# Kernel tuning notes

Hardware: AMD Instinct MI355X
Metric: run time of the kernel (lower is better)

Reference implementation:

```python
import jax, jax.numpy as jnp
import numpy as np

H = 4        # num_heads
R = 5        # dilation_rate
W = 49       # window_size
D = 256      # d_model // 2
B = 32
N = 4900     # must be divisible by W*R = 245


def setup_inputs() -> dict:
    key = jax.random.key(0)
    k1, k2, k3, k4, k5 = jax.random.split(key, 5)
    s = 1.0 / np.sqrt(D)
    return {
        "emb": jax.random.normal(k1, (B, N, D), dtype=jnp.float32),
        "Wq": jax.random.normal(k2, (D, D), dtype=jnp.float32) * s,
        "bq": jax.random.normal(k3, (D,), dtype=jnp.float32) * s,
        "Wo": jax.random.normal(k4, (D, D), dtype=jnp.float32) * s,
        "bo": jax.random.normal(k5, (D,), dtype=jnp.float32) * s,
    }


def reference(emb, Wq, bq, Wo, bo):
    b, n, d = emb.shape
    dh = d // H
    g = n // (W * R)  # number of segments
    # Original forward uses q_proj for q, k AND v (faithful to source bug).
    q = emb @ Wq.T + bq  # [B, N, D]
    # Dilated local windows: token index = g*(W*R) + i*R + r.
    # Tokens sharing (segment g, dilation offset r) attend densely over i in [0, W).
    x = q.reshape(b, g, W, R, H, dh)
    scale = jnp.asarray(dh, q.dtype) ** -0.5
    scores = jnp.einsum("bgirhd,bgjrhd->bgrhij", x, x) * scale  # [B,G,R,H,W,W]
    attn = jax.nn.softmax(scores, axis=-1)
    out = jnp.einsum("bgrhij,bgjrhd->bgirhd", attn, x)  # [B,G,W,R,H,dh]
    out = out.reshape(b, n, d)
    return out @ Wo.T + bo
```

## Files before the change

kernel.cpp:

```cpp
#include <hip/hip_runtime.h>
#include <hip/hip_bf16.h>
#include <math.h>

#define NH     4
#define RD     5
#define WW     49
#define DM     256
#define BATCH  32
#define NTOK   4900
#define GSEG   20
#define SEG    245

typedef short bf16x8 __attribute__((ext_vector_type(8)));
typedef short bf16x4 __attribute__((ext_vector_type(4)));
typedef float f32x4  __attribute__((ext_vector_type(4)));

__device__ __forceinline__ short f2bf(float f) {
    union { __hip_bfloat16 h; short s; } u;
    u.h = __float2bfloat16(f);
    return u.s;
}

__device__ __forceinline__ void gl_lds16(const void* g, void* l) {
    __builtin_amdgcn_global_load_lds(
        (const __attribute__((address_space(1))) void*)g,
        (__attribute__((address_space(3))) void*)l, 16, 0, 0);
}

__device__ __forceinline__ int qix(int row, int col) {
    return row * 256 + (col ^ ((row & 7) << 3));
}
__device__ __forceinline__ int tix(int d, int j) {
    return 64 * 256 + d * 64 + (j ^ ((d & 7) << 3));
}

__global__ __launch_bounds__(256)
void wcvt(const float* __restrict__ Wq, const float* __restrict__ Wo,
          short* __restrict__ Wqb, short* __restrict__ Wob) {
    int t = blockIdx.x * 256 + threadIdx.x;
    const float* src = (t < 16384) ? Wq : Wo;
    short* dst = (t < 16384) ? Wqb : Wob;
    int i = (t & 16383) * 4;
    float4 v = *(const float4*)(src + i);
    bf16x4 o = { f2bf(v.x), f2bf(v.y), f2bf(v.z), f2bf(v.w) };
    *(bf16x4*)(dst + i) = o;
}

__global__ __launch_bounds__(256, 2)
void fused(const float* __restrict__ emb, const short* __restrict__ Wqb,
           const float* __restrict__ bq, const short* __restrict__ Wob,
           const float* __restrict__ bo, float* __restrict__ out) {
    __shared__ __align__(16) short sm[64 * 256 + 64 * 256];
    float* As = (float*)sm;

    const int tid = threadIdx.x;
    const int wv = tid >> 6, ln = tid & 63, lc = ln & 15, lq = ln >> 4;

    const int bid = blockIdx.x;
    const int b = bid / 100;
    const int rem = bid - b * 100;
    const int g = rem / 5, r = rem - (rem / 5) * 5;
    const size_t tok0 = (size_t)b * NTOK + (size_t)g * SEG + r;
    const int wn = wv * 64;

    for (int p = wv; p < WW; p += 4)
        gl_lds16(emb + (tok0 + (size_t)p * RD) * DM +
                     (size_t)((ln ^ (p & 7)) << 2),
                 (char*)sm + p * 1024);
    __syncthreads();

    f32x4 acc[4][4] = {};
    {
        const short* br[4];
        #pragma unroll
        for (int ni = 0; ni < 4; ni++)
            br[ni] = Wqb + (size_t)(wn + ni * 16 + lc) * DM + lq * 8;
        bf16x8 wb[2][4];
        #pragma unroll
        for (int ni = 0; ni < 4; ni++) wb[0][ni] = *(const bf16x8*)(br[ni]);
        #pragma unroll
        for (int ni = 0; ni < 4; ni++) wb[1][ni] = *(const bf16x8*)(br[ni] + 32);

        #pragma unroll
        for (int ks = 0; ks < 8; ks++) {
            bf16x8 af[4];
            #pragma unroll
            for (int mi = 0; mi < 4; mi++) {
                const int t = mi * 16 + lc;
                const int clo = (ks * 8 + lq * 2) ^ (t & 7);
                float4 lo = *(const float4*)&As[t * 256 + clo * 4];
                float4 hi = *(const float4*)&As[t * 256 + (clo ^ 1) * 4];
                af[mi] = (bf16x8){ f2bf(lo.x), f2bf(lo.y), f2bf(lo.z), f2bf(lo.w),
                                   f2bf(hi.x), f2bf(hi.y), f2bf(hi.z), f2bf(hi.w) };
            }
            #pragma unroll
            for (int mi = 0; mi < 4; mi++)
                #pragma unroll
                for (int ni = 0; ni < 4; ni++)
                    acc[mi][ni] = __builtin_amdgcn_mfma_f32_16x16x32_bf16(
                        af[mi], wb[ks & 1][ni], acc[mi][ni], 0, 0, 0);
            if (ks < 6) {
                #pragma unroll
                for (int ni = 0; ni < 4; ni++)
                    wb[ks & 1][ni] = *(const bf16x8*)(br[ni] + (ks + 2) * 32);
            }
        }
    }
    __syncthreads();

    {
        float bv[4];
        #pragma unroll
        for (int ni = 0; ni < 4; ni++) bv[ni] = bq[wn + ni * 16 + lc];
        #pragma unroll
        for (int mi = 0; mi < 4; mi++)
            #pragma unroll
            for (int rg = 0; rg < 4; rg++) {
                const int t = mi * 16 + lq * 4 + rg;
                #pragma unroll
                for (int ni = 0; ni < 4; ni++) {
                    const int col = wn + ni * 16 + lc;
                    const short s = (t < WW) ? f2bf(acc[mi][ni][rg] + bv[ni])
                                             : (short)0;
                    sm[qix(t, col)] = s;
                    sm[tix(col, t)] = s;
                }
            }
    }
    __syncthreads();

    {
        const int c0 = wn;
        bf16x8 xa[4][2];
        #pragma unroll
        for (int mi = 0; mi < 4; mi++) {
            xa[mi][0] = *(const bf16x8*)&sm[qix(mi * 16 + lc, c0 + lq * 8)];
            xa[mi][1] = *(const bf16x8*)&sm[qix(mi * 16 + lc, c0 + 32 + lq * 8)];
        }
        f32x4 sa[4][4] = {};
        #pragma unroll
        for (int mi = 0; mi < 4; mi++)
            #pragma unroll
            for (int ni = 0; ni < 4; ni++) {
                sa[mi][ni] = __builtin_amdgcn_mfma_f32_16x16x32_bf16(
                    xa[mi][0], xa[ni][0], sa[mi][ni], 0, 0, 0);
                sa[mi][ni] = __builtin_amdgcn_mfma_f32_16x16x32_bf16(
                    xa[mi][1], xa[ni][1], sa[mi][ni], 0, 0, 0);
            }
        #pragma unroll
        for (int mi = 0; mi < 4; mi++)
            #pragma unroll
            for (int ni = 0; ni < 4; ni++)
                #pragma unroll
                for (int rg = 0; rg < 4; rg++)
                    sa[mi][ni][rg] *= 0.125f;

        const int jb = lq * 4;
        #pragma unroll
        for (int ni = 0; ni < 4; ni++) {
            float m = -1e30f;
            #pragma unroll
            for (int mi = 0; mi < 4; mi++)
                #pragma unroll
                for (int rg = 0; rg < 4; rg++) {
                    const float v = (16 * mi + rg + jb < WW) ? sa[mi][ni][rg]
                                                             : -1e30f;
                    m = fmaxf(m, v);
                }
            m = fmaxf(m, __shfl_xor(m, 16));
            m = fmaxf(m, __shfl_xor(m, 32));
            float l_ = 0.f;
            #pragma unroll
            for (int mi = 0; mi < 4; mi++)
                #pragma unroll
                for (int rg = 0; rg < 4; rg++) {
                    const float e = (16 * mi + rg + jb < WW)
                                        ? __expf(sa[mi][ni][rg] - m) : 0.f;
                    sa[mi][ni][rg] = e;
                    l_ += e;
                }
            l_ += __shfl_xor(l_, 16);
            l_ += __shfl_xor(l_, 32);
            const float inv = 1.f / l_;
            const int i = 16 * ni + lc;
            #pragma unroll
            for (int mi = 0; mi < 4; mi++) {
                bf16x4 w = { f2bf(sa[mi][ni][0] * inv), f2bf(sa[mi][ni][1] * inv),
                             f2bf(sa[mi][ni][2] * inv), f2bf(sa[mi][ni][3] * inv) };
                *(bf16x4*)&sm[qix(i, c0 + 16 * mi + jb)] = w;
            }
        }
        bf16x8 pa[4][2], pb[4][2];
        #pragma unroll
        for (int mi = 0; mi < 4; mi++) {
            pa[mi][0] = *(const bf16x8*)&sm[qix(mi * 16 + lc, c0 + lq * 8)];
            pa[mi][1] = *(const bf16x8*)&sm[qix(mi * 16 + lc, c0 + 32 + lq * 8)];
        }
        #pragma unroll
        for (int ni = 0; ni < 4; ni++) {
            pb[ni][0] = *(const bf16x8*)&sm[tix(c0 + ni * 16 + lc, lq * 8)];
            pb[ni][1] = *(const bf16x8*)&sm[tix(c0 + ni * 16 + lc, 32 + lq * 8)];
        }
        f32x4 oa[4][4] = {};
        #pragma unroll
        for (int mi = 0; mi < 4; mi++)
            #pragma unroll
            for (int ni = 0; ni < 4; ni++) {
                oa[mi][ni] = __builtin_amdgcn_mfma_f32_16x16x32_bf16(
                    pa[mi][0], pb[ni][0], oa[mi][ni], 0, 0, 0);
                oa[mi][ni] = __builtin_amdgcn_mfma_f32_16x16x32_bf16(
                    pa[mi][1], pb[ni][1], oa[mi][ni], 0, 0, 0);
            }
        #pragma unroll
        for (int mi = 0; mi < 4; mi++)
            #pragma unroll
            for (int rg = 0; rg < 4; rg++) {
                const int i = mi * 16 + lq * 4 + rg;
                if (i < WW) {
                    #pragma unroll
                    for (int ni = 0; ni < 4; ni++)
                        sm[qix(i, c0 + ni * 16 + lc)] = f2bf(oa[mi][ni][rg]);
                }
            }
    }
    __syncthreads();

    {
        const short* br[4];
        #pragma unroll
        for (int ni = 0; ni < 4; ni++)
            br[ni] = Wob + (size_t)(wn + ni * 16 + lc) * DM + lq * 8;
        int trow[4];
        #pragma unroll
        for (int mi = 0; mi < 4; mi++) {
            int t = mi * 16 + lc;
            trow[mi] = (t > WW - 1) ? (WW - 1) : t;
        }
        f32x4 ac3[4][4] = {};
        bf16x8 wb[2][4];
        #pragma unroll
        for (int ni = 0; ni < 4; ni++) wb[0][ni] = *(const bf16x8*)(br[ni]);
        #pragma unroll
        for (int ni = 0; ni < 4; ni++) wb[1][ni] = *(const bf16x8*)(br[ni] + 32);

        #pragma unroll
        for (int ks = 0; ks < 8; ks++) {
            bf16x8 af[4];
            #pragma unroll
            for (int mi = 0; mi < 4; mi++)
                af[mi] = *(const bf16x8*)&sm[qix(trow[mi], ks * 32 + lq * 8)];
            #pragma unroll
            for (int mi = 0; mi < 4; mi++)
                #pragma unroll
                for (int ni = 0; ni < 4; ni++)
                    ac3[mi][ni] = __builtin_amdgcn_mfma_f32_16x16x32_bf16(
                        af[mi], wb[ks & 1][ni], ac3[mi][ni], 0, 0, 0);
            if (ks < 6) {
                #pragma unroll
                for (int ni = 0; ni < 4; ni++)
                    wb[ks & 1][ni] = *(const bf16x8*)(br[ni] + (ks + 2) * 32);
            }
        }
        float bv[4];
        #pragma unroll
        for (int ni = 0; ni < 4; ni++) bv[ni] = bo[wn + ni * 16 + lc];
        #pragma unroll
        for (int mi = 0; mi < 4; mi++)
            #pragma unroll
            for (int rg = 0; rg < 4; rg++) {
                const int t = mi * 16 + lq * 4 + rg;
                if (t < WW) {
                    float* op = out + (tok0 + (size_t)t * RD) * DM + wn;
                    #pragma unroll
                    for (int ni = 0; ni < 4; ni++)
                        op[ni * 16 + lc] = ac3[mi][ni][rg] + bv[ni];
                }
            }
    }
}

extern "C" void kernel_launch(void* const* d_in, const int* in_sizes, int n_in,
                              void* d_out, int out_size, void* d_ws, size_t ws_size,
                              hipStream_t stream) {
    const float* emb = (const float*)d_in[0];
    const float* Wq  = (const float*)d_in[1];
    const float* bq  = (const float*)d_in[2];
    const float* Wo  = (const float*)d_in[3];
    const float* bo  = (const float*)d_in[4];
    float* out = (float*)d_out;

    short* Wqb = (short*)d_ws;
    short* Wob = Wqb + DM * DM;

    wcvt<<<dim3(128), dim3(256), 0, stream>>>(Wq, Wo, Wqb, Wob);
    fused<<<dim3(BATCH * GSEG * RD), dim3(256), 0, stream>>>(
        emb, Wqb, bq, Wob, bo, out);
}
```

Baseline: 378.7 us.

## Split each block across eight waves by row halves and vectorize transposed stores

Doubles the block to 512 threads so each head's wave pair splits the 64 token rows into two halves. This covers the Q projection, the attention, and the output projection, cutting per-wave accumulator registers and raising wave count per CU. The transposed Q copy now uses a 4-element swizzle so each lane writes one bf16x4 instead of scalar stores. An extra barrier is added before the probability writes overwrite the shared Q rows. Each wave still loads the full weight slices, so global weight traffic per block doubles.

```diff
diff --git a/kernel.cpp b/kernel.cpp
--- a/kernel.cpp
+++ b/kernel.cpp
@@ -10,6 +10,7 @@
 #define NTOK   4900
 #define GSEG   20
 #define SEG    245
+#define XTB    (64 * 256)
 
 typedef short bf16x8 __attribute__((ext_vector_type(8)));
 typedef short bf16x4 __attribute__((ext_vector_type(4)));
@@ -30,8 +31,8 @@
 __device__ __forceinline__ int qix(int row, int col) {
     return row * 256 + (col ^ ((row & 7) << 3));
 }
-__device__ __forceinline__ int tix(int d, int j) {
-    return 64 * 256 + d * 64 + (j ^ ((d & 7) << 3));
+__device__ __forceinline__ int tix4(int d, int j) {
+    return XTB + d * 64 + ((((j >> 2) ^ ((d & 7) << 1)) << 2) | (j & 3));
 }
 
 __global__ __launch_bounds__(256)
@@ -46,30 +47,31 @@
     *(bf16x4*)(dst + i) = o;
 }
 
-__global__ __launch_bounds__(256, 2)
+__global__ __launch_bounds__(512, 4)
 void fused(const float* __restrict__ emb, const short* __restrict__ Wqb,
            const float* __restrict__ bq, const short* __restrict__ Wob,
            const float* __restrict__ bo, float* __restrict__ out) {
-    __shared__ __align__(16) short sm[64 * 256 + 64 * 256];
+    __shared__ __align__(16) short sm[XTB + 64 * 256];
     float* As = (float*)sm;
 
     const int tid = threadIdx.x;
     const int wv = tid >> 6, ln = tid & 63, lc = ln & 15, lq = ln >> 4;
+    const int hd = wv & 3, hf = wv >> 2;
+    const int wn = hd * 64, wm = hf * 32;
 
     const int bid = blockIdx.x;
     const int b = bid / 100;
     const int rem = bid - b * 100;
     const int g = rem / 5, r = rem - (rem / 5) * 5;
     const size_t tok0 = (size_t)b * NTOK + (size_t)g * SEG + r;
-    const int wn = wv * 64;
-
-    for (int p = wv; p < WW; p += 4)
+
+    for (int p = wv; p < WW; p += 8)
         gl_lds16(emb + (tok0 + (size_t)p * RD) * DM +
                      (size_t)((ln ^ (p & 7)) << 2),
                  (char*)sm + p * 1024);
     __syncthreads();
 
-    f32x4 acc[4][4] = {};
+    f32x4 acc[2][4] = {};
     {
         const short* br[4];
         #pragma unroll
@@ -83,10 +85,10 @@
 
         #pragma unroll
         for (int ks = 0; ks < 8; ks++) {
-            bf16x8 af[4];
-            #pragma unroll
-            for (int mi = 0; mi < 4; mi++) {
-                const int t = mi * 16 + lc;
+            bf16x8 af[2];
+            #pragma unroll
+            for (int mi = 0; mi < 2; mi++) {
+                const int t = wm + mi * 16 + lc;
                 const int clo = (ks * 8 + lq * 2) ^ (t & 7);
                 float4 lo = *(const float4*)&As[t * 256 + clo * 4];
                 float4 hi = *(const float4*)&As[t * 256 + (clo ^ 1) * 4];
@@ -94,7 +96,7 @@
                                    f2bf(hi.x), f2bf(hi.y), f2bf(hi.z), f2bf(hi.w) };
             }
             #pragma unroll
-            for (int mi = 0; mi < 4; mi++)
+            for (int mi = 0; mi < 2; mi++)
                 #pragma unroll
                 for (int ni = 0; ni < 4; ni++)
                     acc[mi][ni] = __builtin_amdgcn_mfma_f32_16x16x32_bf16(
@@ -113,113 +115,115 @@
         #pragma unroll
         for (int ni = 0; ni < 4; ni++) bv[ni] = bq[wn + ni * 16 + lc];
         #pragma unroll
-        for (int mi = 0; mi < 4; mi++)
-            #pragma unroll
-            for (int rg = 0; rg < 4; rg++) {
-                const int t = mi * 16 + lq * 4 + rg;
-                #pragma unroll
-                for (int ni = 0; ni < 4; ni++) {
-                    const int col = wn + ni * 16 + lc;
-                    const short s = (t < WW) ? f2bf(acc[mi][ni][rg] + bv[ni])
-                                             : (short)0;
-                    sm[qix(t, col)] = s;
-                    sm[tix(col, t)] = s;
-                }
-            }
+        for (int mi = 0; mi < 2; mi++) {
+            const int t0 = wm + mi * 16 + lq * 4;
+            #pragma unroll
+            for (int ni = 0; ni < 4; ni++) {
+                const int col = wn + ni * 16 + lc;
+                short s[4];
+                #pragma unroll
+                for (int rg = 0; rg < 4; rg++)
+                    s[rg] = (t0 + rg < WW) ? f2bf(acc[mi][ni][rg] + bv[ni])
+                                           : (short)0;
+                #pragma unroll
+                for (int rg = 0; rg < 4; rg++)
+                    sm[qix(t0 + rg, col)] = s[rg];
+                bf16x4 w = { s[0], s[1], s[2], s[3] };
+                *(bf16x4*)&sm[tix4(col, t0)] = w;
+            }
+        }
     }
     __syncthreads();
 
     {
         const int c0 = wn;
-        bf16x8 xa[4][2];
-        #pragma unroll
-        for (int mi = 0; mi < 4; mi++) {
-            xa[mi][0] = *(const bf16x8*)&sm[qix(mi * 16 + lc, c0 + lq * 8)];
-            xa[mi][1] = *(const bf16x8*)&sm[qix(mi * 16 + lc, c0 + 32 + lq * 8)];
-        }
-        f32x4 sa[4][4] = {};
-        #pragma unroll
-        for (int mi = 0; mi < 4; mi++)
-            #pragma unroll
-            for (int ni = 0; ni < 4; ni++) {
-                sa[mi][ni] = __builtin_amdgcn_mfma_f32_16x16x32_bf16(
-                    xa[mi][0], xa[ni][0], sa[mi][ni], 0, 0, 0);
-                sa[mi][ni] = __builtin_amdgcn_mfma_f32_16x16x32_bf16(
-                    xa[mi][1], xa[ni][1], sa[mi][ni], 0, 0, 0);
-            }
-        #pragma unroll
-        for (int mi = 0; mi < 4; mi++)
-            #pragma unroll
-            for (int ni = 0; ni < 4; ni++)
-                #pragma unroll
-                for (int rg = 0; rg < 4; rg++)
-                    sa[mi][ni][rg] *= 0.125f;
+        bf16x8 xa[4][2], xb[2][2];
+        #pragma unroll
+        for (int mj = 0; mj < 4; mj++) {
+            xa[mj][0] = *(const bf16x8*)&sm[qix(mj * 16 + lc, c0 + lq * 8)];
+            xa[mj][1] = *(const bf16x8*)&sm[qix(mj * 16 + lc, c0 + 32 + lq * 8)];
+        }
+        #pragma unroll
+        for (int ni = 0; ni < 2; ni++) {
+            xb[ni][0] = *(const bf16x8*)&sm[qix(wm + ni * 16 + lc, c0 + lq * 8)];
+            xb[ni][1] = *(const bf16x8*)&sm[qix(wm + ni * 16 + lc, c0 + 32 + lq * 8)];
+        }
+        f32x4 sa[4][2] = {};
+        #pragma unroll
+        for (int mj = 0; mj < 4; mj++)
+            #pragma unroll
+            for (int ni = 0; ni < 2; ni++) {
+                sa[mj][ni] = __builtin_amdgcn_mfma_f32_16x16x32_bf16(
+                    xa[mj][0], xb[ni][0], sa[mj][ni], 0, 0, 0);
+                sa[mj][ni] = __builtin_amdgcn_mfma_f32_16x16x32_bf16(
+                    xa[mj][1], xb[ni][1], sa[mj][ni], 0, 0, 0);
+            }
+        __syncthreads();
 
         const int jb = lq * 4;
         #pragma unroll
-        for (int ni = 0; ni < 4; ni++) {
+        for (int ni = 0; ni < 2; ni++) {
             float m = -1e30f;
             #pragma unroll
-            for (int mi = 0; mi < 4; mi++)
+            for (int mj = 0; mj < 4; mj++)
                 #pragma unroll
                 for (int rg = 0; rg < 4; rg++) {
-                    const float v = (16 * mi + rg + jb < WW) ? sa[mi][ni][rg]
-                                                             : -1e30f;
-                    m = fmaxf(m, v);
+                    sa[mj][ni][rg] *= 0.125f;
+                    if (16 * mj + jb + rg < WW) m = fmaxf(m, sa[mj][ni][rg]);
                 }
             m = fmaxf(m, __shfl_xor(m, 16));
             m = fmaxf(m, __shfl_xor(m, 32));
             float l_ = 0.f;
             #pragma unroll
-            for (int mi = 0; mi < 4; mi++)
+            for (int mj = 0; mj < 4; mj++)
                 #pragma unroll
                 for (int rg = 0; rg < 4; rg++) {
-                    const float e = (16 * mi + rg + jb < WW)
-                                        ? __expf(sa[mi][ni][rg] - m) : 0.f;
-                    sa[mi][ni][rg] = e;
+                    const float e = (16 * mj + jb + rg < WW)
+                                        ? __expf(sa[mj][ni][rg] - m) : 0.f;
+                    sa[mj][ni][rg] = e;
                     l_ += e;
                 }
             l_ += __shfl_xor(l_, 16);
             l_ += __shfl_xor(l_, 32);
             const float inv = 1.f / l_;
-            const int i = 16 * ni + lc;
-            #pragma unroll
-            for (int mi = 0; mi < 4; mi++) {
-                bf16x4 w = { f2bf(sa[mi][ni][0] * inv), f2bf(sa[mi][ni][1] * inv),
-                             f2bf(sa[mi][ni][2] * inv), f2bf(sa[mi][ni][3] * inv) };
-                *(bf16x4*)&sm[qix(i, c0 + 16 * mi + jb)] = w;
-            }
-        }
-        bf16x8 pa[4][2], pb[4][2];
-        #pragma unroll
-        for (int mi = 0; mi < 4; mi++) {
-            pa[mi][0] = *(const bf16x8*)&sm[qix(mi * 16 + lc, c0 + lq * 8)];
-            pa[mi][1] = *(const bf16x8*)&sm[qix(mi * 16 + lc, c0 + 32 + lq * 8)];
-        }
-        #pragma unroll
-        for (int ni = 0; ni < 4; ni++) {
-            pb[ni][0] = *(const bf16x8*)&sm[tix(c0 + ni * 16 + lc, lq * 8)];
-            pb[ni][1] = *(const bf16x8*)&sm[tix(c0 + ni * 16 + lc, 32 + lq * 8)];
-        }
-        f32x4 oa[4][4] = {};
-        #pragma unroll
-        for (int mi = 0; mi < 4; mi++)
-            #pragma unroll
-            for (int ni = 0; ni < 4; ni++) {
-                oa[mi][ni] = __builtin_amdgcn_mfma_f32_16x16x32_bf16(
-                    pa[mi][0], pb[ni][0], oa[mi][ni], 0, 0, 0);
-                oa[mi][ni] = __builtin_amdgcn_mfma_f32_16x16x32_bf16(
-                    pa[mi][1], pb[ni][1], oa[mi][ni], 0, 0, 0);
-            }
-        #pragma unroll
-        for (int mi = 0; mi < 4; mi++)
+            const int i = wm + ni * 16 + lc;
+            #pragma unroll
+            for (int mj = 0; mj < 4; mj++) {
+                bf16x4 pw = { f2bf(sa[mj][ni][0] * inv), f2bf(sa[mj][ni][1] * inv),
+                              f2bf(sa[mj][ni][2] * inv), f2bf(sa[mj][ni][3] * inv) };
+                *(bf16x4*)&sm[qix(i, c0 + 16 * mj + jb)] = pw;
+            }
+        }
+        bf16x8 pa[2][2], pb[4][2];
+        #pragma unroll
+        for (int ni = 0; ni < 2; ni++) {
+            pa[ni][0] = *(const bf16x8*)&sm[qix(wm + ni * 16 + lc, c0 + lq * 8)];
+            pa[ni][1] = *(const bf16x8*)&sm[qix(wm + ni * 16 + lc, c0 + 32 + lq * 8)];
+        }
+        #pragma unroll
+        for (int nd = 0; nd < 4; nd++) {
+            pb[nd][0] = *(const bf16x8*)&sm[tix4(c0 + nd * 16 + lc, lq * 8)];
+            pb[nd][1] = *(const bf16x8*)&sm[tix4(c0 + nd * 16 + lc, 32 + lq * 8)];
+        }
+        f32x4 oa[2][4] = {};
+        #pragma unroll
+        for (int ni = 0; ni < 2; ni++)
+            #pragma unroll
+            for (int nd = 0; nd < 4; nd++) {
+                oa[ni][nd] = __builtin_amdgcn_mfma_f32_16x16x32_bf16(
+                    pa[ni][0], pb[nd][0], oa[ni][nd], 0, 0, 0);
+                oa[ni][nd] = __builtin_amdgcn_mfma_f32_16x16x32_bf16(
+                    pa[ni][1], pb[nd][1], oa[ni][nd], 0, 0, 0);
+            }
+        #pragma unroll
+        for (int ni = 0; ni < 2; ni++)
             #pragma unroll
             for (int rg = 0; rg < 4; rg++) {
-                const int i = mi * 16 + lq * 4 + rg;
+                const int i = wm + ni * 16 + lq * 4 + rg;
                 if (i < WW) {
                     #pragma unroll
-                    for (int ni = 0; ni < 4; ni++)
-                        sm[qix(i, c0 + ni * 16 + lc)] = f2bf(oa[mi][ni][rg]);
+                    for (int nd = 0; nd < 4; nd++)
+                        sm[qix(i, c0 + nd * 16 + lc)] = f2bf(oa[ni][nd][rg]);
                 }
             }
     }
@@ -230,13 +234,13 @@
         #pragma unroll
         for (int ni = 0; ni < 4; ni++)
             br[ni] = Wob + (size_t)(wn + ni * 16 + lc) * DM + lq * 8;
-        int trow[4];
-        #pragma unroll
-        for (int mi = 0; mi < 4; mi++) {
-            int t = mi * 16 + lc;
+        int trow[2];
+        #pragma unroll
+        for (int mi = 0; mi < 2; mi++) {
+            int t = wm + mi * 16 + lc;
             trow[mi] = (t > WW - 1) ? (WW - 1) : t;
         }
-        f32x4 ac3[4][4] = {};
+        f32x4 ac3[2][4] = {};
         bf16x8 wb[2][4];
         #pragma unroll
         for (int ni = 0; ni < 4; ni++) wb[0][ni] = *(const bf16x8*)(br[ni]);
@@ -245,12 +249,12 @@
 
         #pragma unroll
         for (int ks = 0; ks < 8; ks++) {
-            bf16x8 af[4];
-            #pragma unroll
-            for (int mi = 0; mi < 4; mi++)
+            bf16x8 af[2];
+            #pragma unroll
+            for (int mi = 0; mi < 2; mi++)
                 af[mi] = *(const bf16x8*)&sm[qix(trow[mi], ks * 32 + lq * 8)];
             #pragma unroll
-            for (int mi = 0; mi < 4; mi++)
+            for (int mi = 0; mi < 2; mi++)
                 #pragma unroll
                 for (int ni = 0; ni < 4; ni++)
                     ac3[mi][ni] = __builtin_amdgcn_mfma_f32_16x16x32_bf16(
@@ -265,10 +269,10 @@
         #pragma unroll
         for (int ni = 0; ni < 4; ni++) bv[ni] = bo[wn + ni * 16 + lc];
         #pragma unroll
-        for (int mi = 0; mi < 4; mi++)
+        for (int mi = 0; mi < 2; mi++)
             #pragma unroll
             for (int rg = 0; rg < 4; rg++) {
-                const int t = mi * 16 + lq * 4 + rg;
+                const int t = wm + mi * 16 + lq * 4 + rg;
                 if (t < WW) {
                     float* op = out + (tok0 + (size_t)t * RD) * DM + wn;
                     #pragma unroll
@@ -293,6 +297,6 @@
     short* Wob = Wqb + DM * DM;
 
     wcvt<<<dim3(128), dim3(256), 0, stream>>>(Wq, Wo, Wqb, Wob);
-    fused<<<dim3(BATCH * GSEG * RD), dim3(256), 0, stream>>>(
+    fused<<<dim3(BATCH * GSEG * RD), dim3(512), 0, stream>>>(
         emb, Wqb, bq, Wob, bo, out);
 }
```

After: 435.2 us. 1.15x slower.
